# Performance work log

Hardware: AMD Instinct MI355X
Metric: run time of the kernel (lower is better)

Reference implementation:

```python
import jax, jax.numpy as jnp
import numpy as np

N = 50000   # nodes
E = 800000  # edges
F_IN, F_HID, F_OUT = 128, 96, 40


def setup_inputs() -> dict:
    key = jax.random.key(0)
    ks = jax.random.split(key, 9)
    x = jax.random.normal(ks[0], (N, F_IN), dtype=jnp.float32)
    edge_index = jax.random.randint(ks[1], (2, E), 0, N, dtype=jnp.int32)
    def lin(k, fi, fo):
        s = 1.0 / np.sqrt(fi)
        return jax.random.uniform(k, (fi, fo), jnp.float32, -s, s)
    W1 = lin(ks[2], F_IN, F_HID)
    b1 = jnp.zeros((F_HID,), jnp.float32)
    W2 = lin(ks[3], F_HID, F_HID)
    b2 = jnp.zeros((F_HID,), jnp.float32)
    Wout = lin(ks[4], F_HID, F_OUT)
    bout = jnp.zeros((F_OUT,), jnp.float32)
    return {"x": x, "edge_index": edge_index, "W1": W1, "b1": b1,
            "W2": W2, "b2": b2, "Wout": Wout, "bout": bout}


def _gcn_norm(edge_index, n):
    # add self-loops, symmetric degree normalization (PyG GCNConv default)
    loops = jnp.arange(n, dtype=edge_index.dtype)
    src = jnp.concatenate([edge_index[0], loops])
    dst = jnp.concatenate([edge_index[1], loops])
    deg = jax.ops.segment_sum(jnp.ones_like(dst, dtype=jnp.float32), dst,
                              num_segments=n)
    dinv = jnp.where(deg > 0, jax.lax.rsqrt(deg), 0.0)
    norm = dinv[src] * dinv[dst]   # [E+N]
    return src, dst, norm


def _gcn_layer(h, src, dst, norm, W, b, n):
    # linear transform, then normalized scatter-add aggregation, then bias
    h = h @ W                                 # [N, Fout]
    msg = h[src] * norm[:, None]              # gather + scale
    agg = jax.ops.segment_sum(msg, dst, num_segments=n)
    return agg + b


def reference(x, edge_index, W1, b1, W2, b2, Wout, bout):
    n = x.shape[0]
    src, dst, norm = _gcn_norm(edge_index, n)
    h = jax.nn.relu(_gcn_layer(x, src, dst, norm, W1, b1, n))
    h = jax.nn.relu(_gcn_layer(h, src, dst, norm, W2, b2, n))
    return h @ Wout + bout
```

## Files before the change

kernel.cpp:

```cpp
#include <hip/hip_runtime.h>
#include <hip/hip_fp16.h>

#define N_NODES 50000
#define N_EDGES 800000
#define F_INN   128
#define F_HID   96
#define F_OUTT  40

typedef _Float16 half8 __attribute__((ext_vector_type(8)));
typedef float    floatx4 __attribute__((ext_vector_type(4)));

template <int FI, typename TIN>
__device__ __forceinline__ void mfma_gemm_body(
        const TIN* __restrict__ X, const __half* __restrict__ BTg,
        float4* __restrict__ Th4, int n, int bx) {
    __shared__ __half BTl[96 * 136];
    __shared__ __half OUTl[4 * 16 * 104];
    int tid = threadIdx.x;
    {
        const int4* s = reinterpret_cast<const int4*>(BTg);
        int4* d = reinterpret_cast<int4*>(BTl);
        for (int i = tid; i < 96 * 136 / 8; i += 256) d[i] = s[i];
    }
    __syncthreads();

    int lane = tid & 63, w = tid >> 6;
    int lm = lane & 15, q = lane >> 4;
    int base = bx * 64 + w * 16;
    int node = base + lm;
    int nclamp = min(node, n - 1);
    const TIN* Xrow = X + (size_t)nclamp * FI;

    floatx4 cf[6];
    #pragma unroll
    for (int t = 0; t < 6; ++t) cf[t] = (floatx4){0.f, 0.f, 0.f, 0.f};

    constexpr int KS = FI / 32;
    #pragma unroll
    for (int ks = 0; ks < KS; ++ks) {
        half8 bv;
        if constexpr (sizeof(TIN) == 4) {
            const float4* xr = reinterpret_cast<const float4*>(Xrow + 32 * ks + q * 8);
            float4 f0 = xr[0], f1 = xr[1];
            union { half8 v; __half2 h[4]; } b;
            b.h[0] = __floats2half2_rn(f0.x, f0.y);
            b.h[1] = __floats2half2_rn(f0.z, f0.w);
            b.h[2] = __floats2half2_rn(f1.x, f1.y);
            b.h[3] = __floats2half2_rn(f1.z, f1.w);
            bv = b.v;
        } else {
            bv = *reinterpret_cast<const half8*>(Xrow + 32 * ks + q * 8);
        }
        #pragma unroll
        for (int t = 0; t < 6; ++t) {
            half8 a = *reinterpret_cast<const half8*>(
                &BTl[(t * 16 + lm) * 136 + q * 8 + 32 * ks]);
            cf[t] = __builtin_amdgcn_mfma_f32_16x16x32_f16(a, bv, cf[t], 0, 0, 0);
        }
    }

    __half* orow = OUTl + (w * 16 + lm) * 104;
    #pragma unroll
    for (int t = 0; t < 6; ++t) {
        union { int2 i2; __half2 h[2]; } u;
        u.h[0] = __floats2half2_rn(cf[t][0], cf[t][1]);
        u.h[1] = __floats2half2_rn(cf[t][2], cf[t][3]);
        *reinterpret_cast<int2*>(&orow[t * 16 + q * 4]) = u.i2;
    }
    #pragma unroll
    for (int R = 0; R < 3; ++R) {
        int nl = lane >> 2, c = (lane & 3) + 4 * R;
        float4 v = *reinterpret_cast<const float4*>(&OUTl[(w * 16 + nl) * 104 + c * 8]);
        int gn = base + nl;
        if (gn < n) Th4[(size_t)gn * 12 + c] = v;
    }
}

__global__ __launch_bounds__(256) void count_gemm1_kernel(
        const int* __restrict__ dst, int* __restrict__ counts4, int* __restrict__ rank,
        int e, const float* __restrict__ X, const __half* __restrict__ BT1,
        float4* __restrict__ Th4, int n, int nCB) {
    if ((int)blockIdx.x < nCB) {
        int i = blockIdx.x * 256 + threadIdx.x;
        if (i < e) rank[i] = atomicAdd(&counts4[dst[i] * 4 + (i & 3)], 1);
    } else {
        mfma_gemm_body<F_INN, float>(X, BT1, Th4, n, blockIdx.x - nCB);
    }
}

template <int FI, typename TIN>
__global__ __launch_bounds__(256) void mfma_gemm_kernel(
        const TIN* __restrict__ X, const __half* __restrict__ BTg,
        float4* __restrict__ Th4, int n) {
    mfma_gemm_body<FI, TIN>(X, BTg, Th4, n, blockIdx.x);
}

__global__ void wt_kernel(const float* __restrict__ W1, const float* __restrict__ W2,
                          __half* __restrict__ BT1, __half* __restrict__ BT2) {
    int i = blockIdx.x * 256 + threadIdx.x;
    if (i < 96 * 128) {
        int j = i / 128, k = i - j * 128;
        BT1[j * 136 + k] = __float2half(W1[k * 96 + j]);
    } else if (i < 96 * 128 + 96 * 96) {
        int t = i - 96 * 128;
        int j = t / 96, k = t - j * 96;
        BT2[j * 136 + k] = __float2half(W2[k * 96 + j]);
    }
}

__global__ __launch_bounds__(1024) void scan_local_kernel(
        const int4* __restrict__ counts4, int* __restrict__ row_start,
        float* __restrict__ dinv, int* __restrict__ blk_sums, int n) {
    __shared__ int wave_sums[16];
    int tid = threadIdx.x, lane = tid & 63, wid = tid >> 6;
    int i = blockIdx.x * 1024 + tid;
    int v = 0;
    if (i < n) {
        int4 c = counts4[i];
        v = c.x + c.y + c.z + c.w;
    }
    int val = v;
    #pragma unroll
    for (int off = 1; off < 64; off <<= 1) {
        int u = __shfl_up(val, off, 64);
        if (lane >= off) val += u;
    }
    if (lane == 63) wave_sums[wid] = val;
    __syncthreads();
    if (wid == 0) {
        int w = (lane < 16) ? wave_sums[lane] : 0;
        #pragma unroll
        for (int off = 1; off < 16; off <<= 1) {
            int u = __shfl_up(w, off, 64);
            if (lane >= off) w += u;
        }
        if (lane < 16) wave_sums[lane] = w;
    }
    __syncthreads();
    int excl = ((wid == 0) ? 0 : wave_sums[wid - 1]) + (val - v);
    if (i < n) {
        row_start[i] = excl;
        dinv[i] = rsqrtf((float)(v + 1));
    }
    if (tid == 0) blk_sums[blockIdx.x] = wave_sums[15];
}

__global__ __launch_bounds__(1024) void scan_apply_kernel(
        int* __restrict__ row_start, const int* __restrict__ blk_sums,
        const int4* __restrict__ counts4, int4* __restrict__ base4, int n, int nblk) {
    __shared__ int s_my, s_tot;
    int tid = threadIdx.x;
    if (tid < 64) {
        int v = (tid < nblk) ? blk_sums[tid] : 0;
        int val = v;
        #pragma unroll
        for (int off = 1; off < 64; off <<= 1) {
            int u = __shfl_up(val, off, 64);
            if (tid >= off) val += u;
        }
        if (tid == (int)blockIdx.x) s_my = val - v;
        if (tid == 63) s_tot = val;
    }
    __syncthreads();
    int i = blockIdx.x * 1024 + tid;
    if (i < n) {
        int4 c = counts4[i];
        int b = row_start[i] + s_my;
        row_start[i] = b;
        base4[i] = make_int4(b, b + c.x, b + c.x + c.y, b + c.x + c.y + c.z);
    }
    if (blockIdx.x == 0 && tid == 0) row_start[n] = s_tot;
}

__global__ void fill_csr_kernel(const int* __restrict__ src, const int* __restrict__ dst,
                                const int* __restrict__ rank, const int* __restrict__ base4,
                                int* __restrict__ csr_src, int e) {
    int i = blockIdx.x * blockDim.x + threadIdx.x;
    if (i >= e) return;
    csr_src[base4[dst[i] * 4 + (i & 3)] + rank[i]] = src[i];
}

__global__ __launch_bounds__(256) void agg_kernel(
        const __half2* __restrict__ T, const int* __restrict__ row_start,
        const int* __restrict__ csr_src, const float* __restrict__ dinv,
        const float* __restrict__ bias, __half2* __restrict__ H, int n) {
    int lane = threadIdx.x & 63;
    int node = __builtin_amdgcn_readfirstlane(blockIdx.x * 4 + (threadIdx.x >> 6));
    if (node >= n) return;
    int fl = min(lane, 47);

    float dn = dinv[node];
    float2 self = __half22float2(T[(size_t)node * 48 + fl]);
    float accx = dn * self.x, accy = dn * self.y;

    int idx = row_start[node];
    int end = row_start[node + 1];
    for (; idx + 8 <= end; idx += 8) {
        int s[8];
        #pragma unroll
        for (int u = 0; u < 8; ++u) s[u] = csr_src[idx + u];
        float ws[8];
        #pragma unroll
        for (int u = 0; u < 8; ++u) ws[u] = dinv[s[u]];
        float2 f[8];
        #pragma unroll
        for (int u = 0; u < 8; ++u) f[u] = __half22float2(T[(size_t)s[u] * 48 + fl]);
        #pragma unroll
        for (int u = 0; u < 8; ++u) {
            accx = fmaf(ws[u], f[u].x, accx);
            accy = fmaf(ws[u], f[u].y, accy);
        }
    }
    for (; idx < end; ++idx) {
        int s = csr_src[idx];
        float w = dinv[s];
        float2 f = __half22float2(T[(size_t)s * 48 + fl]);
        accx = fmaf(w, f.x, accx);
        accy = fmaf(w, f.y, accy);
    }
    if (lane < 48) {
        float2 b = reinterpret_cast<const float2*>(bias)[lane];
        float ox = fmaxf(fmaf(dn, accx, b.x), 0.f);
        float oy = fmaxf(fmaf(dn, accy, b.y), 0.f);
        H[(size_t)node * 48 + lane] = __floats2half2_rn(ox, oy);
    }
}

__global__ __launch_bounds__(320) void gemm_out_kernel(
        const __half2* __restrict__ A, const float* __restrict__ W,
        const float* __restrict__ bias, float* __restrict__ C, int n) {
    __shared__ float Wlds[96 * 40];
    int tid = threadIdx.y * 10 + threadIdx.x;
    for (int i = tid; i < 96 * 10; i += 320)
        reinterpret_cast<float4*>(Wlds)[i] = reinterpret_cast<const float4*>(W)[i];
    __syncthreads();

    int j    = threadIdx.x * 4;
    int node = blockIdx.x * 32 + threadIdx.y;
    int nc   = min(node, n - 1);
    const __half2* Ah = A + (size_t)nc * 48;
    float4 acc = make_float4(0.f, 0.f, 0.f, 0.f);
    for (int k2 = 0; k2 < 48; k2 += 2) {
        float2 a01 = __half22float2(Ah[k2]);
        float2 a23 = __half22float2(Ah[k2 + 1]);
        int k = 2 * k2;
        float4 w0 = *reinterpret_cast<const float4*>(Wlds + (k + 0) * 40 + j);
        float4 w1 = *reinterpret_cast<const float4*>(Wlds + (k + 1) * 40 + j);
        float4 w2 = *reinterpret_cast<const float4*>(Wlds + (k + 2) * 40 + j);
        float4 w3 = *reinterpret_cast<const float4*>(Wlds + (k + 3) * 40 + j);
        acc.x += a01.x * w0.x + a01.y * w1.x + a23.x * w2.x + a23.y * w3.x;
        acc.y += a01.x * w0.y + a01.y * w1.y + a23.x * w2.y + a23.y * w3.y;
        acc.z += a01.x * w0.z + a01.y * w1.z + a23.x * w2.z + a23.y * w3.z;
        acc.w += a01.x * w0.w + a01.y * w1.w + a23.x * w2.w + a23.y * w3.w;
    }
    if (node < n) {
        float4 b = *reinterpret_cast<const float4*>(bias + j);
        acc.x += b.x; acc.y += b.y; acc.z += b.z; acc.w += b.w;
        *reinterpret_cast<float4*>(C + (size_t)node * 40 + j) = acc;
    }
}


extern "C" void kernel_launch(void* const* d_in, const int* in_sizes, int n_in,
                              void* d_out, int out_size, void* d_ws, size_t ws_size,
                              hipStream_t stream) {
    const float* x    = (const float*)d_in[0];
    const int*   ei   = (const int*)d_in[1];
    const float* W1   = (const float*)d_in[2];
    const float* b1   = (const float*)d_in[3];
    const float* W2   = (const float*)d_in[4];
    const float* b2   = (const float*)d_in[5];
    const float* Wout = (const float*)d_in[6];
    const float* bout = (const float*)d_in[7];
    float*       out  = (float*)d_out;

    const int* src = ei;
    const int* dst = ei + N_EDGES;

    char* ws = (char*)d_ws;
    size_t off = 0;
    auto alloc = [&](size_t bytes) {
        size_t o = off;
        off = (off + bytes + 511) & ~(size_t)511;
        return (void*)(ws + o);
    };
    int*     counts4   = (int*)    alloc((size_t)N_NODES * 4 * sizeof(int));
    int4*    base4     = (int4*)   alloc((size_t)N_NODES * sizeof(int4));
    int*     row_start = (int*)    alloc((N_NODES + 1) * sizeof(int));
    float*   dinv      = (float*)  alloc(N_NODES * sizeof(float));
    int*     blk_sums  = (int*)    alloc(64 * sizeof(int));
    int*     rank      = (int*)    alloc((size_t)N_EDGES * sizeof(int));
    int*     csr_src   = (int*)    alloc((size_t)N_EDGES * sizeof(int));
    __half*  BT1       = (__half*) alloc((size_t)96 * 136 * sizeof(__half));
    __half*  BT2       = (__half*) alloc((size_t)96 * 136 * sizeof(__half));
    __half2* Th        = (__half2*)alloc((size_t)N_NODES * 48 * sizeof(__half2));
    __half2* Hh        = (__half2*)alloc((size_t)N_NODES * 48 * sizeof(__half2));

    const int NSCAN = (N_NODES + 1023) / 1024;
    const int CB    = (N_EDGES + 255) / 256;
    const int GB    = (N_NODES + 63) / 64;

    hipMemsetAsync(counts4, 0, (size_t)N_NODES * 4 * sizeof(int), stream);
    wt_kernel<<<(96 * 128 + 96 * 96 + 255) / 256, 256, 0, stream>>>(W1, W2, BT1, BT2);

    count_gemm1_kernel<<<CB + GB, 256, 0, stream>>>(
        dst, counts4, rank, N_EDGES, x, BT1, (float4*)Th, N_NODES, CB);

    scan_local_kernel<<<NSCAN, 1024, 0, stream>>>(
        (const int4*)counts4, row_start, dinv, blk_sums, N_NODES);
    scan_apply_kernel<<<NSCAN, 1024, 0, stream>>>(
        row_start, blk_sums, (const int4*)counts4, base4, N_NODES, NSCAN);
    fill_csr_kernel<<<CB, 256, 0, stream>>>(
        src, dst, rank, (const int*)base4, csr_src, N_EDGES);

    agg_kernel<<<(N_NODES + 3) / 4, 256, 0, stream>>>(
        Th, row_start, csr_src, dinv, b1, Hh, N_NODES);

    mfma_gemm_kernel<F_HID, __half><<<GB, 256, 0, stream>>>(
        (const __half*)Hh, BT2, (float4*)Th, N_NODES);
    agg_kernel<<<(N_NODES + 3) / 4, 256, 0, stream>>>(
        Th, row_start, csr_src, dinv, b2, Hh, N_NODES);

    gemm_out_kernel<<<(N_NODES + 31) / 32, dim3(10, 32), 0, stream>>>(
        Hh, Wout, bout, out, N_NODES);
}
```

Measured before the change: 225.8 us.

## Split count/GEMM1 fusion, fuse memset with weight prep, drop LDS staging in GEMM

Replaces the memset plus weight-transpose launch with a single prep kernel that zeros the counts and converts the weights. Un-fuses the edge-count atomics from the first MFMA GEMM so they run as separate kernels. Removes LDS staging of the transposed weights and of the output tile: the GEMM now reads B fragments straight from global memory (unpadded layout) and writes 8-byte output chunks directly. This saves one launch and shared-memory traffic, at the cost of losing the overlap between atomics and GEMM, and of less coalesced global stores and repeated global weight loads.

```diff
diff --git a/kernel.cpp b/kernel.cpp
--- a/kernel.cpp
+++ b/kernel.cpp
@@ -10,24 +10,116 @@
 typedef _Float16 half8 __attribute__((ext_vector_type(8)));
 typedef float    floatx4 __attribute__((ext_vector_type(4)));
 
+#define ZB 196
+#define WB 84
+
+__global__ __launch_bounds__(256) void prep_kernel(
+        int4* __restrict__ counts4, const float* __restrict__ W1,
+        const float* __restrict__ W2, __half* __restrict__ BT1,
+        __half* __restrict__ BT2) {
+    int b = blockIdx.x;
+    if (b < ZB) {
+        int i = b * 256 + threadIdx.x;
+        if (i < N_NODES) counts4[i] = make_int4(0, 0, 0, 0);
+    } else {
+        int i = (b - ZB) * 256 + threadIdx.x;
+        if (i < 96 * 128) {
+            int j = i / 128, k = i - j * 128;
+            BT1[j * 128 + k] = __float2half(W1[k * 96 + j]);
+        } else if (i < 96 * 128 + 96 * 96) {
+            int t = i - 96 * 128;
+            int j = t / 96, k = t - j * 96;
+            BT2[j * 96 + k] = __float2half(W2[k * 96 + j]);
+        }
+    }
+}
+
+__global__ void count_kernel(const int* __restrict__ dst, int* __restrict__ counts4,
+                             int* __restrict__ rank, int e) {
+    int i = blockIdx.x * blockDim.x + threadIdx.x;
+    if (i < e) rank[i] = atomicAdd(&counts4[dst[i] * 4 + (i & 3)], 1);
+}
+
+__global__ __launch_bounds__(1024) void scan_local_kernel(
+        const int4* __restrict__ counts4, int* __restrict__ row_start,
+        float* __restrict__ dinv, int* __restrict__ blk_sums, int n) {
+    __shared__ int wave_sums[16];
+    int tid = threadIdx.x, lane = tid & 63, wid = tid >> 6;
+    int i = blockIdx.x * 1024 + tid;
+    int v = 0;
+    if (i < n) {
+        int4 c = counts4[i];
+        v = c.x + c.y + c.z + c.w;
+    }
+    int val = v;
+    #pragma unroll
+    for (int off = 1; off < 64; off <<= 1) {
+        int u = __shfl_up(val, off, 64);
+        if (lane >= off) val += u;
+    }
+    if (lane == 63) wave_sums[wid] = val;
+    __syncthreads();
+    if (wid == 0) {
+        int w = (lane < 16) ? wave_sums[lane] : 0;
+        #pragma unroll
+        for (int off = 1; off < 16; off <<= 1) {
+            int u = __shfl_up(w, off, 64);
+            if (lane >= off) w += u;
+        }
+        if (lane < 16) wave_sums[lane] = w;
+    }
+    __syncthreads();
+    int excl = ((wid == 0) ? 0 : wave_sums[wid - 1]) + (val - v);
+    if (i < n) {
+        row_start[i] = excl;
+        dinv[i] = rsqrtf((float)(v + 1));
+    }
+    if (tid == 0) blk_sums[blockIdx.x] = wave_sums[15];
+}
+
+__global__ __launch_bounds__(1024) void scan_apply_kernel(
+        int* __restrict__ row_start, const int* __restrict__ blk_sums,
+        const int4* __restrict__ counts4, int4* __restrict__ base4, int n, int nblk) {
+    __shared__ int s_my, s_tot;
+    int tid = threadIdx.x;
+    if (tid < 64) {
+        int v = (tid < nblk) ? blk_sums[tid] : 0;
+        int val = v;
+        #pragma unroll
+        for (int off = 1; off < 64; off <<= 1) {
+            int u = __shfl_up(val, off, 64);
+            if (tid >= off) val += u;
+        }
+        if (tid == (int)blockIdx.x) s_my = val - v;
+        if (tid == 63) s_tot = val;
+    }
+    __syncthreads();
+    int i = blockIdx.x * 1024 + tid;
+    if (i < n) {
+        int4 c = counts4[i];
+        int b = row_start[i] + s_my;
+        row_start[i] = b;
+        base4[i] = make_int4(b, b + c.x, b + c.x + c.y, b + c.x + c.y + c.z);
+    }
+    if (blockIdx.x == 0 && tid == 0) row_start[n] = s_tot;
+}
+
+__global__ void fill_csr_kernel(const int* __restrict__ src, const int* __restrict__ dst,
+                                const int* __restrict__ rank, const int* __restrict__ base4,
+                                int* __restrict__ csr_src, int e) {
+    int i = blockIdx.x * blockDim.x + threadIdx.x;
+    if (i >= e) return;
+    csr_src[base4[dst[i] * 4 + (i & 3)] + rank[i]] = src[i];
+}
+
 template <int FI, typename TIN>
 __device__ __forceinline__ void mfma_gemm_body(
         const TIN* __restrict__ X, const __half* __restrict__ BTg,
-        float4* __restrict__ Th4, int n, int bx) {
-    __shared__ __half BTl[96 * 136];
-    __shared__ __half OUTl[4 * 16 * 104];
+        __half* __restrict__ Th, int n, int bx) {
     int tid = threadIdx.x;
-    {
-        const int4* s = reinterpret_cast<const int4*>(BTg);
-        int4* d = reinterpret_cast<int4*>(BTl);
-        for (int i = tid; i < 96 * 136 / 8; i += 256) d[i] = s[i];
-    }
-    __syncthreads();
-
     int lane = tid & 63, w = tid >> 6;
     int lm = lane & 15, q = lane >> 4;
-    int base = bx * 64 + w * 16;
-    int node = base + lm;
+    int node = bx * 64 + w * 16 + lm;
     int nclamp = min(node, n - 1);
     const TIN* Xrow = X + (size_t)nclamp * FI;
 
@@ -54,130 +146,28 @@
         #pragma unroll
         for (int t = 0; t < 6; ++t) {
             half8 a = *reinterpret_cast<const half8*>(
-                &BTl[(t * 16 + lm) * 136 + q * 8 + 32 * ks]);
+                BTg + (t * 16 + lm) * FI + 32 * ks + q * 8);
             cf[t] = __builtin_amdgcn_mfma_f32_16x16x32_f16(a, bv, cf[t], 0, 0, 0);
         }
     }
 
-    __half* orow = OUTl + (w * 16 + lm) * 104;
-    #pragma unroll
-    for (int t = 0; t < 6; ++t) {
-        union { int2 i2; __half2 h[2]; } u;
-        u.h[0] = __floats2half2_rn(cf[t][0], cf[t][1]);
-        u.h[1] = __floats2half2_rn(cf[t][2], cf[t][3]);
-        *reinterpret_cast<int2*>(&orow[t * 16 + q * 4]) = u.i2;
-    }
-    #pragma unroll
-    for (int R = 0; R < 3; ++R) {
-        int nl = lane >> 2, c = (lane & 3) + 4 * R;
-        float4 v = *reinterpret_cast<const float4*>(&OUTl[(w * 16 + nl) * 104 + c * 8]);
-        int gn = base + nl;
-        if (gn < n) Th4[(size_t)gn * 12 + c] = v;
-    }
-}
-
-__global__ __launch_bounds__(256) void count_gemm1_kernel(
-        const int* __restrict__ dst, int* __restrict__ counts4, int* __restrict__ rank,
-        int e, const float* __restrict__ X, const __half* __restrict__ BT1,
-        float4* __restrict__ Th4, int n, int nCB) {
-    if ((int)blockIdx.x < nCB) {
-        int i = blockIdx.x * 256 + threadIdx.x;
-        if (i < e) rank[i] = atomicAdd(&counts4[dst[i] * 4 + (i & 3)], 1);
-    } else {
-        mfma_gemm_body<F_INN, float>(X, BT1, Th4, n, blockIdx.x - nCB);
+    if (node < n) {
+        __half* orow = Th + (size_t)node * 96;
+        #pragma unroll
+        for (int t = 0; t < 6; ++t) {
+            union { int2 i2; __half2 h[2]; } u;
+            u.h[0] = __floats2half2_rn(cf[t][0], cf[t][1]);
+            u.h[1] = __floats2half2_rn(cf[t][2], cf[t][3]);
+            *reinterpret_cast<int2*>(orow + t * 16 + q * 4) = u.i2;
+        }
     }
 }
 
 template <int FI, typename TIN>
 __global__ __launch_bounds__(256) void mfma_gemm_kernel(
         const TIN* __restrict__ X, const __half* __restrict__ BTg,
-        float4* __restrict__ Th4, int n) {
-    mfma_gemm_body<FI, TIN>(X, BTg, Th4, n, blockIdx.x);
-}
-
-__global__ void wt_kernel(const float* __restrict__ W1, const float* __restrict__ W2,
-                          __half* __restrict__ BT1, __half* __restrict__ BT2) {
-    int i = blockIdx.x * 256 + threadIdx.x;
-    if (i < 96 * 128) {
-        int j = i / 128, k = i - j * 128;
-        BT1[j * 136 + k] = __float2half(W1[k * 96 + j]);
-    } else if (i < 96 * 128 + 96 * 96) {
-        int t = i - 96 * 128;
-        int j = t / 96, k = t - j * 96;
-        BT2[j * 136 + k] = __float2half(W2[k * 96 + j]);
-    }
-}
-
-__global__ __launch_bounds__(1024) void scan_local_kernel(
-        const int4* __restrict__ counts4, int* __restrict__ row_start,
-        float* __restrict__ dinv, int* __restrict__ blk_sums, int n) {
-    __shared__ int wave_sums[16];
-    int tid = threadIdx.x, lane = tid & 63, wid = tid >> 6;
-    int i = blockIdx.x * 1024 + tid;
-    int v = 0;
-    if (i < n) {
-        int4 c = counts4[i];
-        v = c.x + c.y + c.z + c.w;
-    }
-    int val = v;
-    #pragma unroll
-    for (int off = 1; off < 64; off <<= 1) {
-        int u = __shfl_up(val, off, 64);
-        if (lane >= off) val += u;
-    }
-    if (lane == 63) wave_sums[wid] = val;
-    __syncthreads();
-    if (wid == 0) {
-        int w = (lane < 16) ? wave_sums[lane] : 0;
-        #pragma unroll
-        for (int off = 1; off < 16; off <<= 1) {
-            int u = __shfl_up(w, off, 64);
-            if (lane >= off) w += u;
-        }
-        if (lane < 16) wave_sums[lane] = w;
-    }
-    __syncthreads();
-    int excl = ((wid == 0) ? 0 : wave_sums[wid - 1]) + (val - v);
-    if (i < n) {
-        row_start[i] = excl;
-        dinv[i] = rsqrtf((float)(v + 1));
-    }
-    if (tid == 0) blk_sums[blockIdx.x] = wave_sums[15];
-}
-
-__global__ __launch_bounds__(1024) void scan_apply_kernel(
-        int* __restrict__ row_start, const int* __restrict__ blk_sums,
-        const int4* __restrict__ counts4, int4* __restrict__ base4, int n, int nblk) {
-    __shared__ int s_my, s_tot;
-    int tid = threadIdx.x;
-    if (tid < 64) {
-        int v = (tid < nblk) ? blk_sums[tid] : 0;
-        int val = v;
-        #pragma unroll
-        for (int off = 1; off < 64; off <<= 1) {
-            int u = __shfl_up(val, off, 64);
-            if (tid >= off) val += u;
-        }
-        if (tid == (int)blockIdx.x) s_my = val - v;
-        if (tid == 63) s_tot = val;
-    }
-    __syncthreads();
-    int i = blockIdx.x * 1024 + tid;
-    if (i < n) {
-        int4 c = counts4[i];
-        int b = row_start[i] + s_my;
-        row_start[i] = b;
-        base4[i] = make_int4(b, b + c.x, b + c.x + c.y, b + c.x + c.y + c.z);
-    }
-    if (blockIdx.x == 0 && tid == 0) row_start[n] = s_tot;
-}
-
-__global__ void fill_csr_kernel(const int* __restrict__ src, const int* __restrict__ dst,
-                                const int* __restrict__ rank, const int* __restrict__ base4,
-                                int* __restrict__ csr_src, int e) {
-    int i = blockIdx.x * blockDim.x + threadIdx.x;
-    if (i >= e) return;
-    csr_src[base4[dst[i] * 4 + (i & 3)] + rank[i]] = src[i];
+        __half* __restrict__ Th, int n) {
+    mfma_gemm_body<FI, TIN>(X, BTg, Th, n, blockIdx.x);
 }
 
 __global__ __launch_bounds__(256) void agg_kernel(
@@ -291,20 +281,21 @@
     int*     blk_sums  = (int*)    alloc(64 * sizeof(int));
     int*     rank      = (int*)    alloc((size_t)N_EDGES * sizeof(int));
     int*     csr_src   = (int*)    alloc((size_t)N_EDGES * sizeof(int));
-    __half*  BT1       = (__half*) alloc((size_t)96 * 136 * sizeof(__half));
-    __half*  BT2       = (__half*) alloc((size_t)96 * 136 * sizeof(__half));
-    __half2* Th        = (__half2*)alloc((size_t)N_NODES * 48 * sizeof(__half2));
-    __half2* Hh        = (__half2*)alloc((size_t)N_NODES * 48 * sizeof(__half2));
+    __half*  BT1       = (__half*) alloc((size_t)96 * 128 * sizeof(__half));
+    __half*  BT2       = (__half*) alloc((size_t)96 * 96 * sizeof(__half));
+    __half*  Th        = (__half*) alloc((size_t)N_NODES * 96 * sizeof(__half));
+    __half*  Hh        = (__half*) alloc((size_t)N_NODES * 96 * sizeof(__half));
 
     const int NSCAN = (N_NODES + 1023) / 1024;
     const int CB    = (N_EDGES + 255) / 256;
     const int GB    = (N_NODES + 63) / 64;
 
-    hipMemsetAsync(counts4, 0, (size_t)N_NODES * 4 * sizeof(int), stream);
-    wt_kernel<<<(96 * 128 + 96 * 96 + 255) / 256, 256, 0, stream>>>(W1, W2, BT1, BT2);
-
-    count_gemm1_kernel<<<CB + GB, 256, 0, stream>>>(
-        dst, counts4, rank, N_EDGES, x, BT1, (float4*)Th, N_NODES, CB);
+    prep_kernel<<<ZB + WB, 256, 0, stream>>>(
+        (int4*)counts4, W1, W2, BT1, BT2);
+
+    count_kernel<<<CB, 256, 0, stream>>>(dst, counts4, rank, N_EDGES);
+
+    mfma_gemm_kernel<F_INN, float><<<GB, 256, 0, stream>>>(x, BT1, Th, N_NODES);
 
     scan_local_kernel<<<NSCAN, 1024, 0, stream>>>(
         (const int4*)counts4, row_start, dinv, blk_sums, N_NODES);
@@ -314,13 +305,12 @@
         src, dst, rank, (const int*)base4, csr_src, N_EDGES);
 
     agg_kernel<<<(N_NODES + 3) / 4, 256, 0, stream>>>(
-        Th, row_start, csr_src, dinv, b1, Hh, N_NODES);
-
-    mfma_gemm_kernel<F_HID, __half><<<GB, 256, 0, stream>>>(
-        (const __half*)Hh, BT2, (float4*)Th, N_NODES);
+        (const __half2*)Th, row_start, csr_src, dinv, b1, (__half2*)Hh, N_NODES);
+
+    mfma_gemm_kernel<F_HID, __half><<<GB, 256, 0, stream>>>(Hh, BT2, Th, N_NODES);
     agg_kernel<<<(N_NODES + 3) / 4, 256, 0, stream>>>(
-        Th, row_start, csr_src, dinv, b2, Hh, N_NODES);
+        (const __half2*)Th, row_start, csr_src, dinv, b2, (__half2*)Hh, N_NODES);
 
     gemm_out_kernel<<<(N_NODES + 31) / 32, dim3(10, 32), 0, stream>>>(
-        Hh, Wout, bout, out, N_NODES);
-}
+        (const __half2*)Hh, Wout, bout, out, N_NODES);
+}
```

Result: slower. 238.8 us (+5.8%).

## Fuse second-layer aggregation with output projection into one kernel

Applied to the files above, without the earlier changes.

Replaces the second agg_kernel and the separate gemm_out_kernel with a single agg_out_kernel. Each wave aggregates one node's 96 features, stages the ReLU'd row in LDS, then 40 lanes compute the output projection reading Wout directly from global memory. This removes the write and re-read of the intermediate hidden matrix and one kernel launch. The cost is a serial 96-step per-lane dot product with uncached-in-LDS weight loads at the tail of every wave. The hidden row is also kept in fp32 instead of being rounded to half.

```diff
diff --git a/kernel.cpp b/kernel.cpp
--- a/kernel.cpp
+++ b/kernel.cpp
@@ -226,37 +226,61 @@
     }
 }
 
-__global__ __launch_bounds__(320) void gemm_out_kernel(
-        const __half2* __restrict__ A, const float* __restrict__ W,
-        const float* __restrict__ bias, float* __restrict__ C, int n) {
-    __shared__ float Wlds[96 * 40];
-    int tid = threadIdx.y * 10 + threadIdx.x;
-    for (int i = tid; i < 96 * 10; i += 320)
-        reinterpret_cast<float4*>(Wlds)[i] = reinterpret_cast<const float4*>(W)[i];
-    __syncthreads();
-
-    int j    = threadIdx.x * 4;
-    int node = blockIdx.x * 32 + threadIdx.y;
-    int nc   = min(node, n - 1);
-    const __half2* Ah = A + (size_t)nc * 48;
-    float4 acc = make_float4(0.f, 0.f, 0.f, 0.f);
-    for (int k2 = 0; k2 < 48; k2 += 2) {
-        float2 a01 = __half22float2(Ah[k2]);
-        float2 a23 = __half22float2(Ah[k2 + 1]);
-        int k = 2 * k2;
-        float4 w0 = *reinterpret_cast<const float4*>(Wlds + (k + 0) * 40 + j);
-        float4 w1 = *reinterpret_cast<const float4*>(Wlds + (k + 1) * 40 + j);
-        float4 w2 = *reinterpret_cast<const float4*>(Wlds + (k + 2) * 40 + j);
-        float4 w3 = *reinterpret_cast<const float4*>(Wlds + (k + 3) * 40 + j);
-        acc.x += a01.x * w0.x + a01.y * w1.x + a23.x * w2.x + a23.y * w3.x;
-        acc.y += a01.x * w0.y + a01.y * w1.y + a23.x * w2.y + a23.y * w3.y;
-        acc.z += a01.x * w0.z + a01.y * w1.z + a23.x * w2.z + a23.y * w3.z;
-        acc.w += a01.x * w0.w + a01.y * w1.w + a23.x * w2.w + a23.y * w3.w;
-    }
-    if (node < n) {
-        float4 b = *reinterpret_cast<const float4*>(bias + j);
-        acc.x += b.x; acc.y += b.y; acc.z += b.z; acc.w += b.w;
-        *reinterpret_cast<float4*>(C + (size_t)node * 40 + j) = acc;
+__global__ __launch_bounds__(256) void agg_out_kernel(
+        const __half2* __restrict__ T, const int* __restrict__ row_start,
+        const int* __restrict__ csr_src, const float* __restrict__ dinv,
+        const float* __restrict__ bias,
+        const float* __restrict__ Wout, const float* __restrict__ bout,
+        float* __restrict__ out, int n) {
+    __shared__ float hbuf[4][96];
+    int lane = threadIdx.x & 63;
+    int w    = threadIdx.x >> 6;
+    int node = __builtin_amdgcn_readfirstlane(blockIdx.x * 4 + w);
+    if (node >= n) return;
+    int fl = min(lane, 47);
+
+    float dn = dinv[node];
+    float2 self = __half22float2(T[(size_t)node * 48 + fl]);
+    float accx = dn * self.x, accy = dn * self.y;
+
+    int idx = row_start[node];
+    int end = row_start[node + 1];
+    for (; idx + 8 <= end; idx += 8) {
+        int s[8];
+        #pragma unroll
+        for (int u = 0; u < 8; ++u) s[u] = csr_src[idx + u];
+        float ws[8];
+        #pragma unroll
+        for (int u = 0; u < 8; ++u) ws[u] = dinv[s[u]];
+        float2 f[8];
+        #pragma unroll
+        for (int u = 0; u < 8; ++u) f[u] = __half22float2(T[(size_t)s[u] * 48 + fl]);
+        #pragma unroll
+        for (int u = 0; u < 8; ++u) {
+            accx = fmaf(ws[u], f[u].x, accx);
+            accy = fmaf(ws[u], f[u].y, accy);
+        }
+    }
+    for (; idx < end; ++idx) {
+        int s = csr_src[idx];
+        float wv = dinv[s];
+        float2 f = __half22float2(T[(size_t)s * 48 + fl]);
+        accx = fmaf(wv, f.x, accx);
+        accy = fmaf(wv, f.y, accy);
+    }
+
+    if (lane < 48) {
+        float2 b = reinterpret_cast<const float2*>(bias)[lane];
+        hbuf[w][2 * lane]     = fmaxf(fmaf(dn, accx, b.x), 0.f);
+        hbuf[w][2 * lane + 1] = fmaxf(fmaf(dn, accy, b.y), 0.f);
+    }
+
+    if (lane < 40) {
+        float acc = bout[lane];
+        #pragma unroll 8
+        for (int k = 0; k < 96; ++k)
+            acc = fmaf(hbuf[w][k], Wout[k * 40 + lane], acc);
+        out[(size_t)node * 40 + lane] = acc;
     }
 }
 
@@ -293,8 +317,8 @@
     int*     csr_src   = (int*)    alloc((size_t)N_EDGES * sizeof(int));
     __half*  BT1       = (__half*) alloc((size_t)96 * 136 * sizeof(__half));
     __half*  BT2       = (__half*) alloc((size_t)96 * 136 * sizeof(__half));
-    __half2* Th        = (__half2*)alloc((size_t)N_NODES * 48 * sizeof(__half2));
-    __half2* Hh        = (__half2*)alloc((size_t)N_NODES * 48 * sizeof(__half2));
+    __half*  Th        = (__half*) alloc((size_t)N_NODES * 96 * sizeof(__half));
+    __half*  Hh        = (__half*) alloc((size_t)N_NODES * 96 * sizeof(__half));
 
     const int NSCAN = (N_NODES + 1023) / 1024;
     const int CB    = (N_EDGES + 255) / 256;
@@ -314,13 +338,11 @@
         src, dst, rank, (const int*)base4, csr_src, N_EDGES);
 
     agg_kernel<<<(N_NODES + 3) / 4, 256, 0, stream>>>(
-        Th, row_start, csr_src, dinv, b1, Hh, N_NODES);
+        (const __half2*)Th, row_start, csr_src, dinv, b1, (__half2*)Hh, N_NODES);
 
     mfma_gemm_kernel<F_HID, __half><<<GB, 256, 0, stream>>>(
         (const __half*)Hh, BT2, (float4*)Th, N_NODES);
-    agg_kernel<<<(N_NODES + 3) / 4, 256, 0, stream>>>(
-        Th, row_start, csr_src, dinv, b2, Hh, N_NODES);
-
-    gemm_out_kernel<<<(N_NODES + 31) / 32, dim3(10, 32), 0, stream>>>(
-        Hh, Wout, bout, out, N_NODES);
-}
+
+    agg_out_kernel<<<(N_NODES + 3) / 4, 256, 0, stream>>>(
+        (const __half2*)Th, row_start, csr_src, dinv, b2, Wout, bout, out, N_NODES);
+}
```

Measured after the change: 243.7 us. 1.08x slower.
